# Kernel optimization log

Measured on AMD Instinct MI355X. Metric: run time of the kernel, lower is better.

## Reference

```python
import jax, jax.numpy as jnp
import numpy as np

T, B, E, H, V, L = 64, 64, 512, 1024, 10000, 2


def setup_inputs() -> dict:
    key = jax.random.key(0)
    ks = jax.random.split(key, 24)
    k = 1.0 / np.sqrt(H)
    u = lambda kk, shape, s: jax.random.uniform(kk, shape, jnp.float32, -s, s)
    return {
        "inputs": jax.random.randint(ks[0], (T, B), 0, V, dtype=jnp.int32),
        "hidden": jnp.zeros((L, B, H), jnp.float32),
        "emb": u(ks[1], (V, E), 0.1),
        "Wr0": u(ks[2], (H, E), k),
        "Wz0": u(ks[3], (H, E), k),
        "Wh0": u(ks[4], (H, E), k),
        "WrR": u(ks[5], (L - 1, H, H), k),
        "WzR": u(ks[6], (L - 1, H, H), k),
        "WhR": u(ks[7], (L - 1, H, H), k),
        "brR": u(ks[8], (L - 1, H), k),
        "bzR": u(ks[9], (L - 1, H), k),
        "bhR": u(ks[10], (L - 1, H), k),
        "Ur": u(ks[11], (L, H, H), k),
        "Uz": u(ks[12], (L, H, H), k),
        "Uh": u(ks[13], (L, H, H), k),
        "bur": u(ks[14], (L, H), k),
        "buz": u(ks[15], (L, H), k),
        "buh": u(ks[16], (L, H), k),
        "Wout": u(ks[17], (V, H), 0.1),
        "bout": jnp.zeros((V,), jnp.float32),
    }


def reference(inputs, hidden, emb, Wr0, Wz0, Wh0, WrR, WzR, WhR, brR, bzR, bhR,
              Ur, Uz, Uh, bur, buz, buh, Wout, bout):
    num_layers = hidden.shape[0]
    x_emb = emb[inputs]  # [T, B, E]

    def step(h_prev, x_t):  # h_prev [L,B,H], x_t [B,E]
        x = x_t
        hs = []
        for l in range(num_layers):
            if l == 0:
                rx = x @ Wr0.T  # layer-0 W* have no bias
                zx = x @ Wz0.T
                hx = x @ Wh0.T
            else:
                rx = x @ WrR[l - 1].T + brR[l - 1]
                zx = x @ WzR[l - 1].T + bzR[l - 1]
                hx = x @ WhR[l - 1].T + bhR[l - 1]
            hl = h_prev[l]
            r = jax.nn.sigmoid(rx + hl @ Ur[l].T + bur[l])
            z = jax.nn.sigmoid(zx + hl @ Uz[l].T + buz[l])
            h_tilda = jnp.tanh(hx + (r * hl) @ Uh[l].T + buh[l])
            h_new = (1.0 - z) * hl + z * h_tilda
            hs.append(h_new)
            x = h_new
        logits_t = x @ Wout.T + bout  # [B, V]
        return jnp.stack(hs), logits_t

    h_final, logits = jax.lax.scan(step, hidden, x_emb)
    return logits, h_final  # logits [T,B,V], h_final [L,B,H]
```

## Files before the change

kernel.cpp:

```cpp
#include <hip/hip_runtime.h>
#include <hip/hip_bf16.h>

#define T_ 64
#define B_ 64
#define E_ 512
#define H_ 1024
#define V_ 10000
#define TB 4096
#define BH 65536

typedef unsigned short u16;
typedef unsigned int u32;
typedef unsigned long long u64;
typedef __attribute__((ext_vector_type(8))) short short8v;
typedef __attribute__((ext_vector_type(4))) float f32x4;

__device__ inline f32x4 mfma_bf16(short8v a, short8v b, f32x4 c) {
  return __builtin_amdgcn_mfma_f32_16x16x32_bf16(a, b, c, 0, 0, 0);
}

__device__ inline u16 f2bf(float f) {
  unsigned u = __float_as_uint(f);
  unsigned r = (u + 0x7fffu + ((u >> 16) & 1u)) >> 16;
  return (u16)r;
}
__device__ inline float bf2f(u16 h) { return __uint_as_float(((unsigned)h) << 16); }


__global__ void k_prepall(const float* __restrict__ Wr0, const float* __restrict__ Wz0,
                          const float* __restrict__ Wh0, const float* __restrict__ Ur,
                          const float* __restrict__ Uz, const float* __restrict__ Uh,
                          const float* __restrict__ WrR, const float* __restrict__ WzR,
                          const float* __restrict__ WhR, const float* __restrict__ Wout,
                          u16* __restrict__ W0cat, u16* __restrict__ U0cat,
                          u16* __restrict__ U1W, u16* __restrict__ Woutb) {
  const int HE = H_ * E_;
  const int HH = H_ * H_;
  const size_t n0 = 3u * (size_t)HE;
  const size_t n1 = n0 + 3u * (size_t)HH;
  const size_t n2 = n1 + 3072u * 2048u;
  const size_t n3 = n2 + (size_t)V_ * H_;
  size_t i = (size_t)blockIdx.x * 256 + threadIdx.x;
  const size_t stride = (size_t)gridDim.x * 256;
  for (; i < n3; i += stride) {
    if (i < n0) {
      int g = (int)(i >> 19), off = (int)(i & (HE - 1));
      const float* s = g == 0 ? Wr0 : (g == 1 ? Wz0 : Wh0);
      W0cat[i] = f2bf(s[off]);
    } else if (i < n1) {
      size_t j = i - n0;
      int g = (int)(j >> 20), off = (int)(j & (HH - 1));
      const float* s = g == 0 ? Ur : (g == 1 ? Uz : Uh);
      U0cat[j] = f2bf(s[off]);
    } else if (i < n2) {
      size_t k = i - n1;
      int row = (int)(k >> 11), kk = (int)(k & 2047);
      int g = row >> 10, jj = row & 1023;
      const float* su = g == 0 ? Ur : (g == 1 ? Uz : Uh);
      const float* sw = g == 0 ? WrR : (g == 1 ? WzR : WhR);
      float v = (kk < 1024) ? su[(size_t)HH + (size_t)jj * 1024 + kk]
                            : sw[(size_t)jj * 1024 + (kk - 1024)];
      U1W[k] = f2bf(v);
    } else {
      size_t m = i - n2;
      Woutb[m] = f2bf(Wout[m]);
    }
  }
}

__global__ void k_gather(const int* __restrict__ idx, const float* __restrict__ emb,
                         u16* __restrict__ xbf) {
  int i = blockIdx.x * 256 + threadIdx.x;
  int row = i >> 9, e = i & 511;
  xbf[i] = f2bf(emb[(size_t)idx[row] * E_ + e]);
}

__global__ void k_bias(const float* __restrict__ bur, const float* __restrict__ buz,
                       const float* __restrict__ buh, const float* __restrict__ brR,
                       const float* __restrict__ bzR, const float* __restrict__ bhR,
                       float* __restrict__ bias0, float* __restrict__ bias1) {
  int j = blockIdx.x * 256 + threadIdx.x;
  int seg = j >> 10, col = j & 1023;
  float b0, b1;
  if (seg == 0)      { b0 = bur[col]; b1 = brR[col] + bur[H_ + col]; }
  else if (seg == 1) { b0 = buz[col]; b1 = bzR[col] + buz[H_ + col]; }
  else               { b0 = buh[col]; b1 = bhR[col] + buh[H_ + col]; }
  bias0[j] = b0; bias1[j] = b1;
}

__global__ void k_init(const float* __restrict__ hidden, u16* __restrict__ h0P,
                       u16* __restrict__ h1P) {
  int i = blockIdx.x * 256 + threadIdx.x;
  int row = i >> 10, j = i & 1023;
  int dst = ((j >> 4) << 10) + (row << 4) + (j & 15);
  h0P[dst] = f2bf(hidden[i]);
  h1P[dst] = f2bf(hidden[BH + i]);
}


__global__ __launch_bounds__(256, 2) void k_gemmX(const u16* __restrict__ A,
                                                  const u16* __restrict__ Wt,
                                                  const float* __restrict__ bias,
                                                  u16* __restrict__ XP) {
  const int m0 = blockIdx.x * 128, n0 = blockIdx.y * 128;
  const int wid = threadIdx.x >> 6, lane = threadIdx.x & 63;
  const int wm = wid >> 1, wn = wid & 1;
  const int lrow = lane & 15, lk = (lane >> 4) * 8;
  f32x4 acc[4][4] = {};
  const u16* Ab = A + (size_t)(m0 + wm * 64 + lrow) * 512 + lk;
  const u16* Wb = Wt + (size_t)(n0 + wn * 64 + lrow) * 512 + lk;
  for (int ks = 0; ks < 512; ks += 32) {
    short8v a[4], b[4];
#pragma unroll
    for (int f = 0; f < 4; f++) a[f] = *(const short8v*)(Ab + (size_t)f * 16 * 512 + ks);
#pragma unroll
    for (int f = 0; f < 4; f++) b[f] = *(const short8v*)(Wb + (size_t)f * 16 * 512 + ks);
#pragma unroll
    for (int i = 0; i < 4; i++)
#pragma unroll
      for (int j = 0; j < 4; j++) acc[i][j] = mfma_bf16(a[i], b[j], acc[i][j]);
  }
  const int drow0 = (lane >> 4) * 4, dcol = lane & 15;
#pragma unroll
  for (int i = 0; i < 4; i++)
#pragma unroll
    for (int j = 0; j < 4; j++) {
      int col = n0 + wn * 64 + j * 16 + dcol;
      float bv = bias[col];
      int g = col >> 10, cg = (col & 1023) >> 4, cc = col & 15;
#pragma unroll
      for (int v = 0; v < 4; v++) {
        int row = m0 + wm * 64 + i * 16 + drow0 + v;
        int t = row >> 6, rr = row & 63;
        XP[(((size_t)t * 64 + cg) * 64 + rr) * 48 + g * 16 + cc] = f2bf(acc[i][j][v] + bv);
      }
    }
}


__global__ __launch_bounds__(256, 2) void k_gemmL(const u16* __restrict__ AP,
                                                  const u16* __restrict__ Wt,
                                                  const float* __restrict__ bias,
                                                  float* __restrict__ C) {
  const int xcd = blockIdx.x & 7, idx = blockIdx.x >> 3;
  const int nt = xcd * 10 + (idx % 10);
  const int mt = idx / 10;
  if (nt >= 79) return;
  const int m0 = mt * 128, n0 = nt * 128;
  const int wid = threadIdx.x >> 6, lane = threadIdx.x & 63;
  const int wm = wid >> 1, wn = wid & 1;
  const int lrow = lane & 15, lk = (lane >> 4) * 8;
  const int lkb = lk >> 4, lkc = lk & 15;
  f32x4 acc[4][4] = {};
  const int rowhi = (m0 + wm * 64) >> 6;
  const u16* Ab = AP + (size_t)rowhi * BH + (size_t)lkb * 1024 + lrow * 16 + lkc;
  const u16* Wb = Wt + (size_t)(n0 + wn * 64 + lrow) * 1024 + lk;
  bool nvalid[4];
#pragma unroll
  for (int f = 0; f < 4; f++) nvalid[f] = (n0 + wn * 64 + f * 16 + lrow) < V_;
  const short8v zv = {};
  for (int ks = 0; ks < 1024; ks += 32) {
    short8v a[4], b[4];
#pragma unroll
    for (int f = 0; f < 4; f++) a[f] = *(const short8v*)(Ab + ks * 64 + f * 256);
#pragma unroll
    for (int f = 0; f < 4; f++)
      b[f] = nvalid[f] ? *(const short8v*)(Wb + (size_t)f * 16 * 1024 + ks) : zv;
#pragma unroll
    for (int i = 0; i < 4; i++)
#pragma unroll
      for (int j = 0; j < 4; j++) acc[i][j] = mfma_bf16(a[i], b[j], acc[i][j]);
  }
  const int drow0 = (lane >> 4) * 4, dcol = lane & 15;
#pragma unroll
  for (int i = 0; i < 4; i++)
#pragma unroll
    for (int j = 0; j < 4; j++) {
      int col = n0 + wn * 64 + j * 16 + dcol;
      if (col >= V_) continue;
      float bv = bias[col];
#pragma unroll
      for (int v = 0; v < 4; v++) {
        int row = m0 + wm * 64 + i * 16 + drow0 + v;
        C[(size_t)row * V_ + col] = acc[i][j][v] + bv;
      }
    }
}


__device__ inline void pollall(const int* slots, int tgt) {
  const int lane = threadIdx.x & 63;
  const int* p = slots + lane * 32;
  for (;;) {
    int v = __hip_atomic_load(p, __ATOMIC_RELAXED, __HIP_MEMORY_SCOPE_AGENT);
    if (__all(v >= tgt)) break;
    __builtin_amdgcn_s_sleep(2);
  }
}

__global__ __launch_bounds__(256, 1) void k_recur(
    const u16* __restrict__ U0, const u16* __restrict__ U1W,
    const u16* __restrict__ XP, const float* __restrict__ bias1,
    const float* __restrict__ hidden,
    u16* __restrict__ h0P, u16* __restrict__ h1P,
    u16* __restrict__ r0P, u16* __restrict__ r1P,
    int* __restrict__ flags, float* __restrict__ hfin) {
  __shared__ __align__(16) u16 wlds[65536];

  const int tid = threadIdx.x, gbid = blockIdx.x;
  const int lay = gbid >> 6;
  const int cg = gbid & 63;
  const int jr = cg * 16;
  const int wid = tid >> 6, lane = tid & 63;
  const int lrow = lane & 15, lk = (lane >> 4) * 8;
  const int lk3 = lk >> 3, x7 = lrow & 7;
  const int drow0 = (lane >> 4) * 4, dcol = lane & 15;
  const int abase = (lk >> 4) * 1024 + (wid * 16 + lrow) * 16 + (lk & 15);
  const int KLS = lay ? 11 : 10;
  int* f0s = flags;
  int* f1s = flags + 2048;
  int* myslot = (lay ? f1s : f0s) + cg * 32;

  {
    const u16* Wg = lay ? U1W : U0;
    const int lCPR = lay ? 8 : 7;
    const int NG = lay ? 2 : 3;
    const int total = NG << (4 + lCPR);
    const int KL = 1 << KLS;
    for (int idx = tid; idx < total; idx += 256) {
      int r16 = idx >> lCPR;
      int ch = idx & ((1 << lCPR) - 1);
      int g = r16 >> 4, r = r16 & 15;
      short8v v = *(const short8v*)(Wg + (size_t)((g << 10) + jr + r) * KL + (ch << 3));
      *(short8v*)&wlds[((size_t)r16 << KLS) + ((ch ^ (r & 7)) << 3)] = v;
    }
  }
  __syncthreads();

  const int lbR = lrow << KLS;
  const int lbZ = (16 + lrow) << KLS;
  const int lbH = (32 + lrow) << KLS;
  const u16* Whg = U1W + (size_t)(2048 + jr + lrow) * 2048 + lk;
  const int orow = wid * 16 + drow0;

  float hreg[4];
#pragma unroll
  for (int v = 0; v < 4; v++)
    hreg[v] = hidden[(size_t)lay * BH + (size_t)(orow + v) * 1024 + jr + dcol];

  if (!lay) {
    for (int t = 0; t < T_; t++) {
      float xr[4], xz[4], xh[4], zreg[4];
      const u16* xb = XP + (((size_t)t * 64 + cg) * 64 + orow) * 48 + dcol;
#pragma unroll
      for (int v = 0; v < 4; v++) {
        xr[v] = bf2f(xb[v * 48]);
        xz[v] = bf2f(xb[v * 48 + 16]);
        xh[v] = bf2f(xb[v * 48 + 32]);
      }
      if (t) { if (tid < 64) pollall(f0s, 2 * t); __syncthreads(); }
      f32x4 ar = {}, az = {};
      {
        const u16* Ab = h0P + (size_t)t * BH + abase;
        short8v av[32];
#pragma unroll
        for (int i = 0; i < 32; i++) av[i] = *(const short8v*)(Ab + i * 2048);
#pragma unroll
        for (int i = 0; i < 32; i++) {
          const int sw = (((i * 4) + lk3) ^ x7) << 3;
          ar = mfma_bf16(av[i], *(short8v*)&wlds[lbR + sw], ar);
          az = mfma_bf16(av[i], *(short8v*)&wlds[lbZ + sw], az);
        }
      }
      u16* rtile = r0P + (size_t)t * BH + (size_t)cg * 1024;
#pragma unroll
      for (int v = 0; v < 4; v++) {
        float r = 1.f / (1.f + __expf(-(ar[v] + xr[v])));
        float z = 1.f / (1.f + __expf(-(az[v] + xz[v])));
        zreg[v] = z;
        u16 me = f2bf(r * hreg[v]);
        int oth = __shfl_xor((int)me, 1);
        if (!(dcol & 1)) {
          u32 pk = (u32)me | ((u32)(u16)oth << 16);
          __hip_atomic_store((u32*)(rtile + (orow + v) * 16 + dcol), pk,
                             __ATOMIC_RELAXED, __HIP_MEMORY_SCOPE_AGENT);
        }
      }
      asm volatile("s_waitcnt vmcnt(0)" ::: "memory");
      __syncthreads();
      if (tid == 0)
        __hip_atomic_store(myslot, 2 * t + 1, __ATOMIC_RELAXED, __HIP_MEMORY_SCOPE_AGENT);
      if (tid < 64) pollall(f0s, 2 * t + 1);
      __syncthreads();
      f32x4 ah = {};
      {
        const u16* Abr = r0P + (size_t)t * BH + abase;
        short8v av[32];
#pragma unroll
        for (int i = 0; i < 32; i++) av[i] = *(const short8v*)(Abr + i * 2048);
#pragma unroll
        for (int i = 0; i < 32; i++) {
          const int sw = (((i * 4) + lk3) ^ x7) << 3;
          ah = mfma_bf16(av[i], *(short8v*)&wlds[lbH + sw], ah);
        }
      }
      u16* htile = h0P + (size_t)(t + 1) * BH + (size_t)cg * 1024;
#pragma unroll
      for (int v = 0; v < 4; v++) {
        float th = tanhf(ah[v] + xh[v]);
        float hn = (1.f - zreg[v]) * hreg[v] + zreg[v] * th;
        hreg[v] = hn;
        u16 me = f2bf(hn);
        int oth = __shfl_xor((int)me, 1);
        if (!(dcol & 1)) {
          u32 pk = (u32)me | ((u32)(u16)oth << 16);
          __hip_atomic_store((u32*)(htile + (orow + v) * 16 + dcol), pk,
                             __ATOMIC_RELAXED, __HIP_MEMORY_SCOPE_AGENT);
        }
        if (t == T_ - 1)
          hfin[(size_t)(orow + v) * 1024 + jr + dcol] = hn;
      }
      asm volatile("s_waitcnt vmcnt(0)" ::: "memory");
      __syncthreads();
      if (tid == 0)
        __hip_atomic_store(myslot, 2 * t + 2, __ATOMIC_RELAXED, __HIP_MEMORY_SCOPE_AGENT);
    }
  } else {
    float bR = bias1[jr + dcol];
    float bZ = bias1[1024 + jr + dcol];
    float bH = bias1[2048 + jr + dcol];
    if (tid < 64) pollall(f0s, 2);
    __syncthreads();
    for (int t = 0; t < T_; t++) {
      float zreg[4];
      const u16* Ab0 = h0P + (size_t)(t + 1) * BH + abase;
      f32x4 ar = {}, az = {};
      short8v av0[32];
#pragma unroll
      for (int i = 0; i < 32; i++) av0[i] = *(const short8v*)(Ab0 + i * 2048);
#pragma unroll
      for (int i = 0; i < 32; i++) {
        const int sw = ((128 + i * 4 + lk3) ^ x7) << 3;
        ar = mfma_bf16(av0[i], *(short8v*)&wlds[lbR + sw], ar);
        az = mfma_bf16(av0[i], *(short8v*)&wlds[lbZ + sw], az);
      }
      if (tid < 64) {
        if (t) pollall(f1s, 2 * t);
        int tgt = 2 * (t + 2);
        pollall(f0s, tgt > 2 * T_ ? 2 * T_ : tgt);
      }
      __syncthreads();
      {
        const u16* Ab1 = h1P + (size_t)t * BH + abase;
        short8v av[32];
#pragma unroll
        for (int i = 0; i < 32; i++) av[i] = *(const short8v*)(Ab1 + i * 2048);
#pragma unroll
        for (int i = 0; i < 32; i++) {
          const int sw = ((i * 4 + lk3) ^ x7) << 3;
          ar = mfma_bf16(av[i], *(short8v*)&wlds[lbR + sw], ar);
          az = mfma_bf16(av[i], *(short8v*)&wlds[lbZ + sw], az);
        }
      }
      u16* rtile = r1P + (size_t)t * BH + (size_t)cg * 1024;
#pragma unroll
      for (int v = 0; v < 4; v++) {
        float r = 1.f / (1.f + __expf(-(ar[v] + bR)));
        float z = 1.f / (1.f + __expf(-(az[v] + bZ)));
        zreg[v] = z;
        u16 me = f2bf(r * hreg[v]);
        int oth = __shfl_xor((int)me, 1);
        if (!(dcol & 1)) {
          u32 pk = (u32)me | ((u32)(u16)oth << 16);
          __hip_atomic_store((u32*)(rtile + (orow + v) * 16 + dcol), pk,
                             __ATOMIC_RELAXED, __HIP_MEMORY_SCOPE_AGENT);
        }
      }
      asm volatile("s_waitcnt vmcnt(0)" ::: "memory");
      __syncthreads();
      if (tid == 0)
        __hip_atomic_store(myslot, 2 * t + 1, __ATOMIC_RELAXED, __HIP_MEMORY_SCOPE_AGENT);
      f32x4 ah = {};
#pragma unroll
      for (int i = 0; i < 32; i++)
        ah = mfma_bf16(av0[i], *(const short8v*)(Whg + 1024 + i * 32), ah);
      if (tid < 64) pollall(f1s, 2 * t + 1);
      __syncthreads();
      {
        const u16* Abr = r1P + (size_t)t * BH + abase;
        short8v av[32];
#pragma unroll
        for (int i = 0; i < 32; i++) av[i] = *(const short8v*)(Abr + i * 2048);
#pragma unroll
        for (int i = 0; i < 32; i++)
          ah = mfma_bf16(av[i], *(const short8v*)(Whg + i * 32), ah);
      }
      u16* htile = h1P + (size_t)(t + 1) * BH + (size_t)cg * 1024;
#pragma unroll
      for (int v = 0; v < 4; v++) {
        float th = tanhf(ah[v] + bH);
        float hn = (1.f - zreg[v]) * hreg[v] + zreg[v] * th;
        hreg[v] = hn;
        u16 me = f2bf(hn);
        int oth = __shfl_xor((int)me, 1);
        if (!(dcol & 1)) {
          u32 pk = (u32)me | ((u32)(u16)oth << 16);
          __hip_atomic_store((u32*)(htile + (orow + v) * 16 + dcol), pk,
                             __ATOMIC_RELAXED, __HIP_MEMORY_SCOPE_AGENT);
        }
        if (t == T_ - 1)
          hfin[(size_t)BH + (size_t)(orow + v) * 1024 + jr + dcol] = hn;
      }
      asm volatile("s_waitcnt vmcnt(0)" ::: "memory");
      __syncthreads();
      if (tid == 0)
        __hip_atomic_store(myslot, 2 * t + 2, __ATOMIC_RELAXED, __HIP_MEMORY_SCOPE_AGENT);
    }
  }
}


extern "C" void kernel_launch(void* const* d_in, const int* in_sizes, int n_in,
                              void* d_out, int out_size, void* d_ws, size_t ws_size,
                              hipStream_t stream) {
  const int* inputs = (const int*)d_in[0];
  const float* hidden = (const float*)d_in[1];
  const float* emb = (const float*)d_in[2];
  const float* Wr0 = (const float*)d_in[3];
  const float* Wz0 = (const float*)d_in[4];
  const float* Wh0 = (const float*)d_in[5];
  const float* WrR = (const float*)d_in[6];
  const float* WzR = (const float*)d_in[7];
  const float* WhR = (const float*)d_in[8];
  const float* brR = (const float*)d_in[9];
  const float* bzR = (const float*)d_in[10];
  const float* bhR = (const float*)d_in[11];
  const float* Ur = (const float*)d_in[12];
  const float* Uz = (const float*)d_in[13];
  const float* Uh = (const float*)d_in[14];
  const float* bur = (const float*)d_in[15];
  const float* buz = (const float*)d_in[16];
  const float* buh = (const float*)d_in[17];
  const float* Wout = (const float*)d_in[18];
  const float* bout = (const float*)d_in[19];
  float* out = (float*)d_out;

  char* ws = (char*)d_ws;
  size_t off = 0;
  auto alloc = [&](size_t bytes) -> void* {
    void* p = ws + off;
    off += (bytes + 255) & ~(size_t)255;
    return p;
  };
  u16* x_bf  = (u16*)alloc((size_t)TB * E_ * 2);
  u16* W0cat = (u16*)alloc((size_t)3072 * 512 * 2);
  u16* U0cat = (u16*)alloc((size_t)3072 * 1024 * 2);
  u16* U1W   = (u16*)alloc((size_t)3072 * 2048 * 2);
  u16* Woutb = (u16*)alloc((size_t)V_ * H_ * 2);
  float* bias0 = (float*)alloc(3072 * 4);
  float* bias1 = (float*)alloc(3072 * 4);
  u16* XP    = (u16*)alloc((size_t)TB * 3072 * 2);
  u16* h0P   = (u16*)alloc((size_t)(T_ + 1) * BH * 2);
  u16* h1P   = (u16*)alloc((size_t)(T_ + 1) * BH * 2);
  u16* r0P   = (u16*)alloc((size_t)T_ * BH * 2);
  u16* r1P   = (u16*)alloc((size_t)T_ * BH * 2);
  int* flags = (int*)alloc(32768);
  (void)ws_size; (void)in_sizes; (void)n_in; (void)out_size;

  hipMemsetAsync(flags, 0, 32768, stream);

  k_prepall<<<2048, 256, 0, stream>>>(Wr0, Wz0, Wh0, Ur, Uz, Uh, WrR, WzR, WhR, Wout,
                                      W0cat, U0cat, U1W, Woutb);
  k_gather<<<TB * E_ / 256, 256, 0, stream>>>(inputs, emb, x_bf);
  k_bias<<<12, 256, 0, stream>>>(bur, buz, buh, brR, bzR, bhR, bias0, bias1);
  k_init<<<256, 256, 0, stream>>>(hidden, h0P, h1P);

  k_gemmX<<<dim3(32, 24), 256, 0, stream>>>(x_bf, W0cat, bias0, XP);
  k_recur<<<128, 256, 0, stream>>>(U0cat, U1W, XP, bias1, hidden, h0P, h1P,
                                   r0P, r1P, flags, out + (size_t)TB * V_);
  k_gemmL<<<2560, 256, 0, stream>>>(h1P + BH, Woutb, bout, out);
}
```

Before: 1.389 ms.

## Fuse prep kernels and reorder recurrence to shorten the critical path

Merges the gather, bias, and hidden-init kernels into the single weight-prep kernel, which removes three launches. In the recurrent kernel, only the r-gate MFMAs run before r is published; the z-gate work and the prefetch of the next step's X projections move off that critical path. Layer 1 double-buffers the layer-0 hidden operand across steps, and the two flag polls are split across two waves so they can proceed in parallel. The poll sleep interval is also shortened, and together these add register pressure.

Result: slower. 1.658 ms (+19.3%).

```diff
diff --git a/kernel.cpp b/kernel.cpp
--- a/kernel.cpp
+++ b/kernel.cpp
@@ -27,22 +27,33 @@
 __device__ inline float bf2f(u16 h) { return __uint_as_float(((unsigned)h) << 16); }
 
 
-__global__ void k_prepall(const float* __restrict__ Wr0, const float* __restrict__ Wz0,
-                          const float* __restrict__ Wh0, const float* __restrict__ Ur,
-                          const float* __restrict__ Uz, const float* __restrict__ Uh,
-                          const float* __restrict__ WrR, const float* __restrict__ WzR,
-                          const float* __restrict__ WhR, const float* __restrict__ Wout,
-                          u16* __restrict__ W0cat, u16* __restrict__ U0cat,
-                          u16* __restrict__ U1W, u16* __restrict__ Woutb) {
+__global__ void k_prep(const float* __restrict__ Wr0, const float* __restrict__ Wz0,
+                       const float* __restrict__ Wh0, const float* __restrict__ Ur,
+                       const float* __restrict__ Uz, const float* __restrict__ Uh,
+                       const float* __restrict__ WrR, const float* __restrict__ WzR,
+                       const float* __restrict__ WhR, const float* __restrict__ Wout,
+                       const int* __restrict__ idx, const float* __restrict__ emb,
+                       const float* __restrict__ bur, const float* __restrict__ buz,
+                       const float* __restrict__ buh, const float* __restrict__ brR,
+                       const float* __restrict__ bzR, const float* __restrict__ bhR,
+                       const float* __restrict__ hidden,
+                       u16* __restrict__ W0cat, u16* __restrict__ U0cat,
+                       u16* __restrict__ U1W, u16* __restrict__ Woutb,
+                       u16* __restrict__ x_bf, float* __restrict__ bias0,
+                       float* __restrict__ bias1, u16* __restrict__ h0P,
+                       u16* __restrict__ h1P) {
   const int HE = H_ * E_;
   const int HH = H_ * H_;
   const size_t n0 = 3u * (size_t)HE;
   const size_t n1 = n0 + 3u * (size_t)HH;
   const size_t n2 = n1 + 3072u * 2048u;
   const size_t n3 = n2 + (size_t)V_ * H_;
+  const size_t n4 = n3 + (size_t)TB * E_;
+  const size_t n5 = n4 + 3072;
+  const size_t n6 = n5 + 65536;
   size_t i = (size_t)blockIdx.x * 256 + threadIdx.x;
   const size_t stride = (size_t)gridDim.x * 256;
-  for (; i < n3; i += stride) {
+  for (; i < n6; i += stride) {
     if (i < n0) {
       int g = (int)(i >> 19), off = (int)(i & (HE - 1));
       const float* s = g == 0 ? Wr0 : (g == 1 ? Wz0 : Wh0);
@@ -61,40 +72,29 @@
       float v = (kk < 1024) ? su[(size_t)HH + (size_t)jj * 1024 + kk]
                             : sw[(size_t)jj * 1024 + (kk - 1024)];
       U1W[k] = f2bf(v);
-    } else {
+    } else if (i < n3) {
       size_t m = i - n2;
       Woutb[m] = f2bf(Wout[m]);
+    } else if (i < n4) {
+      size_t j = i - n3;
+      int row = (int)(j >> 9), e = (int)(j & 511);
+      x_bf[j] = f2bf(emb[(size_t)idx[row] * E_ + e]);
+    } else if (i < n5) {
+      int j = (int)(i - n4);
+      int seg = j >> 10, col = j & 1023;
+      float b0, b1;
+      if (seg == 0)      { b0 = bur[col]; b1 = brR[col] + bur[H_ + col]; }
+      else if (seg == 1) { b0 = buz[col]; b1 = bzR[col] + buz[H_ + col]; }
+      else               { b0 = buh[col]; b1 = bhR[col] + buh[H_ + col]; }
+      bias0[j] = b0; bias1[j] = b1;
+    } else {
+      int j = (int)(i - n5);
+      int row = j >> 10, c = j & 1023;
+      int dst = ((c >> 4) << 10) + (row << 4) + (c & 15);
+      h0P[dst] = f2bf(hidden[j]);
+      h1P[dst] = f2bf(hidden[BH + j]);
     }
   }
-}
-
-__global__ void k_gather(const int* __restrict__ idx, const float* __restrict__ emb,
-                         u16* __restrict__ xbf) {
-  int i = blockIdx.x * 256 + threadIdx.x;
-  int row = i >> 9, e = i & 511;
-  xbf[i] = f2bf(emb[(size_t)idx[row] * E_ + e]);
-}
-
-__global__ void k_bias(const float* __restrict__ bur, const float* __restrict__ buz,
-                       const float* __restrict__ buh, const float* __restrict__ brR,
-                       const float* __restrict__ bzR, const float* __restrict__ bhR,
-                       float* __restrict__ bias0, float* __restrict__ bias1) {
-  int j = blockIdx.x * 256 + threadIdx.x;
-  int seg = j >> 10, col = j & 1023;
-  float b0, b1;
-  if (seg == 0)      { b0 = bur[col]; b1 = brR[col] + bur[H_ + col]; }
-  else if (seg == 1) { b0 = buz[col]; b1 = bzR[col] + buz[H_ + col]; }
-  else               { b0 = buh[col]; b1 = bhR[col] + buh[H_ + col]; }
-  bias0[j] = b0; bias1[j] = b1;
-}
-
-__global__ void k_init(const float* __restrict__ hidden, u16* __restrict__ h0P,
-                       u16* __restrict__ h1P) {
-  int i = blockIdx.x * 256 + threadIdx.x;
-  int row = i >> 10, j = i & 1023;
-  int dst = ((j >> 4) << 10) + (row << 4) + (j & 15);
-  h0P[dst] = f2bf(hidden[i]);
-  h1P[dst] = f2bf(hidden[BH + i]);
 }
 
 
@@ -194,7 +194,7 @@
   for (;;) {
     int v = __hip_atomic_load(p, __ATOMIC_RELAXED, __HIP_MEMORY_SCOPE_AGENT);
     if (__all(v >= tgt)) break;
-    __builtin_amdgcn_s_sleep(2);
+    __builtin_amdgcn_s_sleep(1);
   }
 }
 
@@ -249,35 +249,35 @@
     hreg[v] = hidden[(size_t)lay * BH + (size_t)(orow + v) * 1024 + jr + dcol];
 
   if (!lay) {
-    for (int t = 0; t < T_; t++) {
-      float xr[4], xz[4], xh[4], zreg[4];
-      const u16* xb = XP + (((size_t)t * 64 + cg) * 64 + orow) * 48 + dcol;
+    float xr[4], xz[4], xh[4];
+    {
+      const u16* xb = XP + (((size_t)0 * 64 + cg) * 64 + orow) * 48 + dcol;
 #pragma unroll
       for (int v = 0; v < 4; v++) {
         xr[v] = bf2f(xb[v * 48]);
         xz[v] = bf2f(xb[v * 48 + 16]);
         xh[v] = bf2f(xb[v * 48 + 32]);
       }
-      if (t) { if (tid < 64) pollall(f0s, 2 * t); __syncthreads(); }
-      f32x4 ar = {}, az = {};
+    }
+    for (int t = 0; t < T_; t++) {
+      float zreg[4];
+      if (t) { if (wid == 0) pollall(f0s, 2 * t); __syncthreads(); }
+      short8v av[32];
       {
         const u16* Ab = h0P + (size_t)t * BH + abase;
-        short8v av[32];
 #pragma unroll
         for (int i = 0; i < 32; i++) av[i] = *(const short8v*)(Ab + i * 2048);
-#pragma unroll
-        for (int i = 0; i < 32; i++) {
-          const int sw = (((i * 4) + lk3) ^ x7) << 3;
-          ar = mfma_bf16(av[i], *(short8v*)&wlds[lbR + sw], ar);
-          az = mfma_bf16(av[i], *(short8v*)&wlds[lbZ + sw], az);
-        }
+      }
+      f32x4 ar = {};
+#pragma unroll
+      for (int i = 0; i < 32; i++) {
+        const int sw = (((i * 4) + lk3) ^ x7) << 3;
+        ar = mfma_bf16(av[i], *(short8v*)&wlds[lbR + sw], ar);
       }
       u16* rtile = r0P + (size_t)t * BH + (size_t)cg * 1024;
 #pragma unroll
       for (int v = 0; v < 4; v++) {
         float r = 1.f / (1.f + __expf(-(ar[v] + xr[v])));
-        float z = 1.f / (1.f + __expf(-(az[v] + xz[v])));
-        zreg[v] = z;
         u16 me = f2bf(r * hreg[v]);
         int oth = __shfl_xor((int)me, 1);
         if (!(dcol & 1)) {
@@ -290,18 +290,37 @@
       __syncthreads();
       if (tid == 0)
         __hip_atomic_store(myslot, 2 * t + 1, __ATOMIC_RELAXED, __HIP_MEMORY_SCOPE_AGENT);
-      if (tid < 64) pollall(f0s, 2 * t + 1);
+      f32x4 az = {};
+#pragma unroll
+      for (int i = 0; i < 32; i++) {
+        const int sw = (((i * 4) + lk3) ^ x7) << 3;
+        az = mfma_bf16(av[i], *(short8v*)&wlds[lbZ + sw], az);
+      }
+#pragma unroll
+      for (int v = 0; v < 4; v++) zreg[v] = 1.f / (1.f + __expf(-(az[v] + xz[v])));
+      float nxr[4], nxz[4], nxh[4];
+      {
+        int tn = t + 1 < T_ ? t + 1 : T_ - 1;
+        const u16* xb = XP + (((size_t)tn * 64 + cg) * 64 + orow) * 48 + dcol;
+#pragma unroll
+        for (int v = 0; v < 4; v++) {
+          nxr[v] = bf2f(xb[v * 48]);
+          nxz[v] = bf2f(xb[v * 48 + 16]);
+          nxh[v] = bf2f(xb[v * 48 + 32]);
+        }
+      }
+      if (wid == 0) pollall(f0s, 2 * t + 1);
       __syncthreads();
       f32x4 ah = {};
       {
         const u16* Abr = r0P + (size_t)t * BH + abase;
-        short8v av[32];
-#pragma unroll
-        for (int i = 0; i < 32; i++) av[i] = *(const short8v*)(Abr + i * 2048);
+        short8v avr[32];
+#pragma unroll
+        for (int i = 0; i < 32; i++) avr[i] = *(const short8v*)(Abr + i * 2048);
 #pragma unroll
         for (int i = 0; i < 32; i++) {
           const int sw = (((i * 4) + lk3) ^ x7) << 3;
-          ah = mfma_bf16(av[i], *(short8v*)&wlds[lbH + sw], ah);
+          ah = mfma_bf16(avr[i], *(short8v*)&wlds[lbH + sw], ah);
         }
       }
       u16* htile = h0P + (size_t)(t + 1) * BH + (size_t)cg * 1024;
@@ -324,50 +343,53 @@
       __syncthreads();
       if (tid == 0)
         __hip_atomic_store(myslot, 2 * t + 2, __ATOMIC_RELAXED, __HIP_MEMORY_SCOPE_AGENT);
+#pragma unroll
+      for (int v = 0; v < 4; v++) { xr[v] = nxr[v]; xz[v] = nxz[v]; xh[v] = nxh[v]; }
     }
   } else {
     float bR = bias1[jr + dcol];
     float bZ = bias1[1024 + jr + dcol];
     float bH = bias1[2048 + jr + dcol];
-    if (tid < 64) pollall(f0s, 2);
+    if (wid == 0) pollall(f0s, 2);
     __syncthreads();
-    for (int t = 0; t < T_; t++) {
+    short8v avA[32], avB[32];
+    {
+      const u16* Ab = h0P + (size_t)1 * BH + abase;
+#pragma unroll
+      for (int i = 0; i < 32; i++) avA[i] = *(const short8v*)(Ab + i * 2048);
+    }
+
+    auto body = [&](int t, short8v (&avIn)[32], short8v (&avOut)[32]) {
       float zreg[4];
-      const u16* Ab0 = h0P + (size_t)(t + 1) * BH + abase;
       f32x4 ar = {}, az = {};
-      short8v av0[32];
-#pragma unroll
-      for (int i = 0; i < 32; i++) av0[i] = *(const short8v*)(Ab0 + i * 2048);
 #pragma unroll
       for (int i = 0; i < 32; i++) {
         const int sw = ((128 + i * 4 + lk3) ^ x7) << 3;
-        ar = mfma_bf16(av0[i], *(short8v*)&wlds[lbR + sw], ar);
-        az = mfma_bf16(av0[i], *(short8v*)&wlds[lbZ + sw], az);
-      }
-      if (tid < 64) {
+        ar = mfma_bf16(avIn[i], *(short8v*)&wlds[lbR + sw], ar);
+        az = mfma_bf16(avIn[i], *(short8v*)&wlds[lbZ + sw], az);
+      }
+      if (wid == 0) {
         if (t) pollall(f1s, 2 * t);
+      } else if (wid == 1) {
         int tgt = 2 * (t + 2);
         pollall(f0s, tgt > 2 * T_ ? 2 * T_ : tgt);
       }
       __syncthreads();
+      short8v av1[32];
       {
         const u16* Ab1 = h1P + (size_t)t * BH + abase;
-        short8v av[32];
-#pragma unroll
-        for (int i = 0; i < 32; i++) av[i] = *(const short8v*)(Ab1 + i * 2048);
-#pragma unroll
-        for (int i = 0; i < 32; i++) {
-          const int sw = ((i * 4 + lk3) ^ x7) << 3;
-          ar = mfma_bf16(av[i], *(short8v*)&wlds[lbR + sw], ar);
-          az = mfma_bf16(av[i], *(short8v*)&wlds[lbZ + sw], az);
-        }
+#pragma unroll
+        for (int i = 0; i < 32; i++) av1[i] = *(const short8v*)(Ab1 + i * 2048);
+      }
+#pragma unroll
+      for (int i = 0; i < 32; i++) {
+        const int sw = ((i * 4 + lk3) ^ x7) << 3;
+        ar = mfma_bf16(av1[i], *(short8v*)&wlds[lbR + sw], ar);
       }
       u16* rtile = r1P + (size_t)t * BH + (size_t)cg * 1024;
 #pragma unroll
       for (int v = 0; v < 4; v++) {
         float r = 1.f / (1.f + __expf(-(ar[v] + bR)));
-        float z = 1.f / (1.f + __expf(-(az[v] + bZ)));
-        zreg[v] = z;
         u16 me = f2bf(r * hreg[v]);
         int oth = __shfl_xor((int)me, 1);
         if (!(dcol & 1)) {
@@ -380,20 +402,33 @@
       __syncthreads();
       if (tid == 0)
         __hip_atomic_store(myslot, 2 * t + 1, __ATOMIC_RELAXED, __HIP_MEMORY_SCOPE_AGENT);
+#pragma unroll
+      for (int i = 0; i < 32; i++) {
+        const int sw = ((i * 4 + lk3) ^ x7) << 3;
+        az = mfma_bf16(av1[i], *(short8v*)&wlds[lbZ + sw], az);
+      }
+#pragma unroll
+      for (int v = 0; v < 4; v++) zreg[v] = 1.f / (1.f + __expf(-(az[v] + bZ)));
       f32x4 ah = {};
 #pragma unroll
       for (int i = 0; i < 32; i++)
-        ah = mfma_bf16(av0[i], *(const short8v*)(Whg + 1024 + i * 32), ah);
-      if (tid < 64) pollall(f1s, 2 * t + 1);
+        ah = mfma_bf16(avIn[i], *(const short8v*)(Whg + 1024 + i * 32), ah);
+      {
+        int ts = t + 2 < 64 ? t + 2 : 64;
+        const u16* An = h0P + (size_t)ts * BH + abase;
+#pragma unroll
+        for (int i = 0; i < 32; i++) avOut[i] = *(const short8v*)(An + i * 2048);
+      }
+      if (wid == 0) pollall(f1s, 2 * t + 1);
       __syncthreads();
       {
         const u16* Abr = r1P + (size_t)t * BH + abase;
-        short8v av[32];
-#pragma unroll
-        for (int i = 0; i < 32; i++) av[i] = *(const short8v*)(Abr + i * 2048);
+        short8v avr[32];
+#pragma unroll
+        for (int i = 0; i < 32; i++) avr[i] = *(const short8v*)(Abr + i * 2048);
 #pragma unroll
         for (int i = 0; i < 32; i++)
-          ah = mfma_bf16(av[i], *(const short8v*)(Whg + i * 32), ah);
+          ah = mfma_bf16(avr[i], *(const short8v*)(Whg + i * 32), ah);
       }
       u16* htile = h1P + (size_t)(t + 1) * BH + (size_t)cg * 1024;
 #pragma unroll
@@ -415,6 +450,11 @@
       __syncthreads();
       if (tid == 0)
         __hip_atomic_store(myslot, 2 * t + 2, __ATOMIC_RELAXED, __HIP_MEMORY_SCOPE_AGENT);
+    };
+
+    for (int t = 0; t < T_; t += 2) {
+      body(t, avA, avB);
+      body(t + 1, avB, avA);
     }
   }
 }
@@ -469,12 +509,10 @@
 
   hipMemsetAsync(flags, 0, 32768, stream);
 
-  k_prepall<<<2048, 256, 0, stream>>>(Wr0, Wz0, Wh0, Ur, Uz, Uh, WrR, WzR, WhR, Wout,
-                                      W0cat, U0cat, U1W, Woutb);
-  k_gather<<<TB * E_ / 256, 256, 0, stream>>>(inputs, emb, x_bf);
-  k_bias<<<12, 256, 0, stream>>>(bur, buz, buh, brR, bzR, bhR, bias0, bias1);
-  k_init<<<256, 256, 0, stream>>>(hidden, h0P, h1P);
-
+  k_prep<<<2048, 256, 0, stream>>>(Wr0, Wz0, Wh0, Ur, Uz, Uh, WrR, WzR, WhR, Wout,
+                                   inputs, emb, bur, buz, buh, brR, bzR, bhR, hidden,
+                                   W0cat, U0cat, U1W, Woutb, x_bf, bias0, bias1,
+                                   h0P, h1P);
   k_gemmX<<<dim3(32, 24), 256, 0, stream>>>(x_bf, W0cat, bias0, XP);
   k_recur<<<128, 256, 0, stream>>>(U0cat, U1W, XP, bias1, hidden, h0P, h1P,
                                    r0P, r1P, flags, out + (size_t)TB * V_);
```
